# Performance work log

Measured on AMD Instinct MI355X. Metric: run time of the kernel, lower is better.

The kernel has to match this reference:

```python
import jax, jax.numpy as jnp
import numpy as np

ALPHA = 0.2      # LeakyReLU negative slope (hardcoded in StateNetwork: GAT(..., 0.2, 1))
MASK_FILL = 9e-15  # value used for non-edges BEFORE softmax (not -inf, per original code)

N_ENT = 4096     # len(vocab_kge): number of KG entities / GAT nodes
EMB = 64         # embedding_size == gat_emb_size
NHID = 3         # hardcoded in StateNetwork: GAT(gat_emb_size, 3, ...)
BATCH = 4        # number of graphs in graph_rep


def setup_inputs() -> dict:
    key = jax.random.key(0)
    k_adj, k_emb, k_W, k_a, k_fw, k_fb = jax.random.split(key, 6)
    adj = jax.random.randint(k_adj, (BATCH, N_ENT, N_ENT), 0, 2, dtype=jnp.int32)
    ent_emb = jax.random.normal(k_emb, (N_ENT, EMB), dtype=jnp.float32)
    W = jax.random.normal(k_W, (EMB, NHID), dtype=jnp.float32)
    a = jax.random.normal(k_a, (2 * NHID, 1), dtype=jnp.float32)
    fc1_w = jax.random.normal(k_fw, (100, N_ENT * NHID), dtype=jnp.float32) * 0.02
    fc1_b = jax.random.normal(k_fb, (100,), dtype=jnp.float32)
    return {"adj": adj, "ent_emb": ent_emb, "W": W, "a": a, "fc1_w": fc1_w, "fc1_b": fc1_b}


def reference(adj, ent_emb, W, a, fc1_w, fc1_b):
    # GAT layer over the shared entity-embedding node features (same for all graphs).
    h = ent_emb @ W                                   # [N, F]
    F_out = h.shape[1]
    # Pairwise concat score decomposes: e[i,j] = leakyrelu(a1.h_i + a2.h_j)
    src = h @ a[:F_out]                                # [N, 1]
    dst = h @ a[F_out:]                                # [N, 1]
    e = jax.nn.leaky_relu(src + dst.T, negative_slope=ALPHA)   # [N, N]
    # Masked softmax with 9e-15 fill (faithful to torch.where(adj>0, e, 9e-15))
    att = jnp.where(adj > 0, e[None, :, :], jnp.float32(MASK_FILL))  # [B, N, N]
    att = jax.nn.softmax(att, axis=-1)
    h_prime = jnp.einsum('bij,jf->bif', att, h)        # [B, N, F]
    x = jax.nn.elu(h_prime)                            # concat=True -> ELU
    x = x.reshape(adj.shape[0], -1)                    # [B, N*F]
    return x @ fc1_w.T + fc1_b                         # [B, 100]
```

## Files before the change

kernel.cpp:

```cpp
#include <hip/hip_runtime.h>
#include <math.h>

#define N_ENT 4096
#define BATCH 4
#define NHID  3
#define EMB   64
#define ALPHA 0.2f
#define MASK_FILL 9e-15f

__global__ __launch_bounds__(256) void prep_kernel(
    const float* __restrict__ emb, const float* __restrict__ W,
    const float* __restrict__ a,
    float* __restrict__ h0G, float* __restrict__ h1G, float* __restrict__ h2G,
    float* __restrict__ dstG, float* __restrict__ srcG)
{
    int j = blockIdx.x * 256 + threadIdx.x;
    if (j >= N_ENT) return;
    const float* er = emb + (size_t)j * EMB;
    float h0 = 0.f, h1 = 0.f, h2 = 0.f;
    #pragma unroll
    for (int e = 0; e < EMB; ++e) {
        float v = er[e];
        h0 += v * W[e * 3 + 0];
        h1 += v * W[e * 3 + 1];
        h2 += v * W[e * 3 + 2];
    }
    h0G[j] = h0; h1G[j] = h1; h2G[j] = h2;
    srcG[j] = h0 * a[0] + h1 * a[1] + h2 * a[2];
    dstG[j] = h0 * a[3] + h1 * a[4] + h2 * a[5];
}

__global__ __launch_bounds__(256, 2) void gat_row_kernel(
    const int* __restrict__ adj,
    const float* __restrict__ h0G, const float* __restrict__ h1G,
    const float* __restrict__ h2G, const float* __restrict__ dstG,
    const float* __restrict__ srcG, float* __restrict__ xG)
{
    __shared__ float dstL[N_ENT];
    __shared__ float h0L[N_ENT];
    __shared__ float h1L[N_ENT];
    __shared__ float h2L[N_ENT];

    int tid = threadIdx.x;
    for (int t = tid; t < N_ENT; t += 256) {
        dstL[t] = dstG[t];
        h0L[t]  = h0G[t];
        h1L[t]  = h1G[t];
        h2L[t]  = h2G[t];
    }
    __syncthreads();

    int lane = tid & 63;
    int gw   = blockIdx.x * 4 + (tid >> 6);

    for (int r = 0; r < 8; ++r) {
        int row = gw * 8 + r;
        int i   = row & (N_ENT - 1);
        float src = srcG[i];
        const int4* arow = (const int4*)(adj + (size_t)row * N_ENT);

        int4 av[16];
        #pragma unroll
        for (int c = 0; c < 16; ++c) av[c] = arow[c * 64 + lane];

        float vals[64];
        float m = -3.4e38f;
        #pragma unroll
        for (int c = 0; c < 16; ++c) {
            int jb = (c * 64 + lane) * 4;
            float4 d4 = *(const float4*)&dstL[jb];
            float t0 = src + d4.x, t1 = src + d4.y, t2 = src + d4.z, t3 = src + d4.w;
            float v0 = av[c].x > 0 ? fmaxf(t0, ALPHA * t0) : MASK_FILL;
            float v1 = av[c].y > 0 ? fmaxf(t1, ALPHA * t1) : MASK_FILL;
            float v2 = av[c].z > 0 ? fmaxf(t2, ALPHA * t2) : MASK_FILL;
            float v3 = av[c].w > 0 ? fmaxf(t3, ALPHA * t3) : MASK_FILL;
            vals[c * 4 + 0] = v0; vals[c * 4 + 1] = v1;
            vals[c * 4 + 2] = v2; vals[c * 4 + 3] = v3;
            m = fmaxf(m, fmaxf(fmaxf(v0, v1), fmaxf(v2, v3)));
        }
        #pragma unroll
        for (int off = 32; off; off >>= 1)
            m = fmaxf(m, __shfl_xor(m, off, 64));

        float l = 0.f, n0 = 0.f, n1 = 0.f, n2 = 0.f;
        #pragma unroll
        for (int c = 0; c < 16; ++c) {
            int jb = (c * 64 + lane) * 4;
            float4 a0 = *(const float4*)&h0L[jb];
            float4 a1 = *(const float4*)&h1L[jb];
            float4 a2 = *(const float4*)&h2L[jb];
            float p0 = __expf(vals[c * 4 + 0] - m);
            float p1 = __expf(vals[c * 4 + 1] - m);
            float p2 = __expf(vals[c * 4 + 2] - m);
            float p3 = __expf(vals[c * 4 + 3] - m);
            l  += (p0 + p1) + (p2 + p3);
            n0 += p0 * a0.x + p1 * a0.y + p2 * a0.z + p3 * a0.w;
            n1 += p0 * a1.x + p1 * a1.y + p2 * a1.z + p3 * a1.w;
            n2 += p0 * a2.x + p1 * a2.y + p2 * a2.z + p3 * a2.w;
        }
        #pragma unroll
        for (int off = 32; off; off >>= 1) {
            l  += __shfl_xor(l,  off, 64);
            n0 += __shfl_xor(n0, off, 64);
            n1 += __shfl_xor(n1, off, 64);
            n2 += __shfl_xor(n2, off, 64);
        }

        if (lane == 0) {
            float inv = 1.f / l;
            float hp0 = n0 * inv, hp1 = n1 * inv, hp2 = n2 * inv;
            float* xp = xG + (size_t)row * 3;
            xp[0] = hp0 > 0.f ? hp0 : expm1f(hp0);
            xp[1] = hp1 > 0.f ? hp1 : expm1f(hp1);
            xp[2] = hp2 > 0.f ? hp2 : expm1f(hp2);
        }
    }
}

__global__ __launch_bounds__(256) void fc_kernel(
    const float* __restrict__ xG, const float* __restrict__ w,
    const float* __restrict__ bias, float* __restrict__ out)
{
    int k   = blockIdx.x;
    int tid = threadIdx.x;
    const float4* wr = (const float4*)(w + (size_t)k * (N_ENT * NHID));
    const float4* x0 = (const float4*)(xG + 0 * (N_ENT * NHID));
    const float4* x1 = (const float4*)(xG + 1 * (N_ENT * NHID));
    const float4* x2 = (const float4*)(xG + 2 * (N_ENT * NHID));
    const float4* x3 = (const float4*)(xG + 3 * (N_ENT * NHID));

    float acc0 = 0.f, acc1 = 0.f, acc2 = 0.f, acc3 = 0.f;
    for (int t = tid; t < (N_ENT * NHID / 4); t += 256) {
        float4 wv = wr[t];
        float4 xv;
        xv = x0[t]; acc0 += wv.x*xv.x + wv.y*xv.y + wv.z*xv.z + wv.w*xv.w;
        xv = x1[t]; acc1 += wv.x*xv.x + wv.y*xv.y + wv.z*xv.z + wv.w*xv.w;
        xv = x2[t]; acc2 += wv.x*xv.x + wv.y*xv.y + wv.z*xv.z + wv.w*xv.w;
        xv = x3[t]; acc3 += wv.x*xv.x + wv.y*xv.y + wv.z*xv.z + wv.w*xv.w;
    }

    #pragma unroll
    for (int off = 32; off; off >>= 1) {
        acc0 += __shfl_xor(acc0, off, 64);
        acc1 += __shfl_xor(acc1, off, 64);
        acc2 += __shfl_xor(acc2, off, 64);
        acc3 += __shfl_xor(acc3, off, 64);
    }

    __shared__ float red[4][4];
    int lane = tid & 63, wv_ = tid >> 6;
    if (lane == 0) {
        red[wv_][0] = acc0; red[wv_][1] = acc1;
        red[wv_][2] = acc2; red[wv_][3] = acc3;
    }
    __syncthreads();
    if (tid < 4) {
        float s = red[0][tid] + red[1][tid] + red[2][tid] + red[3][tid] + bias[k];
        out[tid * 100 + k] = s;
    }
}

extern "C" void kernel_launch(void* const* d_in, const int* in_sizes, int n_in,
                              void* d_out, int out_size, void* d_ws, size_t ws_size,
                              hipStream_t stream)
{
    const int*   adj  = (const int*)d_in[0];
    const float* emb  = (const float*)d_in[1];
    const float* W    = (const float*)d_in[2];
    const float* a    = (const float*)d_in[3];
    const float* fc1w = (const float*)d_in[4];
    const float* fc1b = (const float*)d_in[5];
    float* out = (float*)d_out;

    float* ws   = (float*)d_ws;
    float* h0G  = ws;
    float* h1G  = ws + 4096;
    float* h2G  = ws + 8192;
    float* dstG = ws + 12288;
    float* srcG = ws + 16384;
    float* xG   = ws + 20480;

    prep_kernel<<<N_ENT / 256, 256, 0, stream>>>(emb, W, a, h0G, h1G, h2G, dstG, srcG);
    gat_row_kernel<<<512, 256, 0, stream>>>(adj, h0G, h1G, h2G, dstG, srcG, xG);
    fc_kernel<<<100, 256, 0, stream>>>(xG, fc1w, fc1b, out);
}
```

Before: 429.4 us.

## Replace two-pass masked softmax with single-pass online softmax per row

Switches the per-row softmax from a max pass followed by an exp/accumulate pass to an online softmax that rescales the running sum and numerators per chunk, then merges the per-lane (m, l, n) states across the wavefront with shuffles. This removes the 64-float vals array and the 16 int4 adjacency registers held across passes, which cuts register pressure. The cost is one extra exp and four rescales per chunk, plus extra exps in the cross-lane reduction. Adjacency loads are no longer all issued up front, so less memory-level parallelism is exposed per wave.

Result: faster. 410.0 us (-4.5%).

```diff
diff --git a/kernel.cpp b/kernel.cpp
--- a/kernel.cpp
+++ b/kernel.cpp
@@ -59,51 +59,54 @@
         float src = srcG[i];
         const int4* arow = (const int4*)(adj + (size_t)row * N_ENT);
 
-        int4 av[16];
-        #pragma unroll
-        for (int c = 0; c < 16; ++c) av[c] = arow[c * 64 + lane];
+        float m = -3.4e38f, l = 0.f, n0 = 0.f, n1 = 0.f, n2 = 0.f;
 
-        float vals[64];
-        float m = -3.4e38f;
-        #pragma unroll
+        #pragma unroll 4
         for (int c = 0; c < 16; ++c) {
+            int4 av = arow[c * 64 + lane];
             int jb = (c * 64 + lane) * 4;
             float4 d4 = *(const float4*)&dstL[jb];
+
             float t0 = src + d4.x, t1 = src + d4.y, t2 = src + d4.z, t3 = src + d4.w;
-            float v0 = av[c].x > 0 ? fmaxf(t0, ALPHA * t0) : MASK_FILL;
-            float v1 = av[c].y > 0 ? fmaxf(t1, ALPHA * t1) : MASK_FILL;
-            float v2 = av[c].z > 0 ? fmaxf(t2, ALPHA * t2) : MASK_FILL;
-            float v3 = av[c].w > 0 ? fmaxf(t3, ALPHA * t3) : MASK_FILL;
-            vals[c * 4 + 0] = v0; vals[c * 4 + 1] = v1;
-            vals[c * 4 + 2] = v2; vals[c * 4 + 3] = v3;
-            m = fmaxf(m, fmaxf(fmaxf(v0, v1), fmaxf(v2, v3)));
-        }
-        #pragma unroll
-        for (int off = 32; off; off >>= 1)
-            m = fmaxf(m, __shfl_xor(m, off, 64));
+            float v0 = av.x > 0 ? fmaxf(t0, ALPHA * t0) : MASK_FILL;
+            float v1 = av.y > 0 ? fmaxf(t1, ALPHA * t1) : MASK_FILL;
+            float v2 = av.z > 0 ? fmaxf(t2, ALPHA * t2) : MASK_FILL;
+            float v3 = av.w > 0 ? fmaxf(t3, ALPHA * t3) : MASK_FILL;
 
-        float l = 0.f, n0 = 0.f, n1 = 0.f, n2 = 0.f;
-        #pragma unroll
-        for (int c = 0; c < 16; ++c) {
-            int jb = (c * 64 + lane) * 4;
+            float m4 = fmaxf(fmaxf(v0, v1), fmaxf(v2, v3));
+            float mn = fmaxf(m, m4);
+            float s  = __expf(m - mn);
+            l *= s; n0 *= s; n1 *= s; n2 *= s;
+            m = mn;
+
             float4 a0 = *(const float4*)&h0L[jb];
             float4 a1 = *(const float4*)&h1L[jb];
             float4 a2 = *(const float4*)&h2L[jb];
-            float p0 = __expf(vals[c * 4 + 0] - m);
-            float p1 = __expf(vals[c * 4 + 1] - m);
-            float p2 = __expf(vals[c * 4 + 2] - m);
-            float p3 = __expf(vals[c * 4 + 3] - m);
+            float p0 = __expf(v0 - m);
+            float p1 = __expf(v1 - m);
+            float p2 = __expf(v2 - m);
+            float p3 = __expf(v3 - m);
             l  += (p0 + p1) + (p2 + p3);
             n0 += p0 * a0.x + p1 * a0.y + p2 * a0.z + p3 * a0.w;
             n1 += p0 * a1.x + p1 * a1.y + p2 * a1.z + p3 * a1.w;
             n2 += p0 * a2.x + p1 * a2.y + p2 * a2.z + p3 * a2.w;
         }
+
         #pragma unroll
         for (int off = 32; off; off >>= 1) {
-            l  += __shfl_xor(l,  off, 64);
-            n0 += __shfl_xor(n0, off, 64);
-            n1 += __shfl_xor(n1, off, 64);
-            n2 += __shfl_xor(n2, off, 64);
+            float mo = __shfl_xor(m,  off, 64);
+            float lo = __shfl_xor(l,  off, 64);
+            float o0 = __shfl_xor(n0, off, 64);
+            float o1 = __shfl_xor(n1, off, 64);
+            float o2 = __shfl_xor(n2, off, 64);
+            float mm = fmaxf(m, mo);
+            float sa = __expf(m  - mm);
+            float sb = __expf(mo - mm);
+            l  = l  * sa + lo * sb;
+            n0 = n0 * sa + o0 * sb;
+            n1 = n1 * sa + o1 * sb;
+            n2 = n2 * sa + o2 * sb;
+            m  = mm;
         }
 
         if (lane == 0) {
```

## Replace two-pass softmax with single-pass bound-max and exp2, widen blocks

Applied to the files above, without the earlier changes.

Instead of computing each row's exact max over the masked scores, the kernel takes an upper bound from the global max of dst (leaky-relu is monotonic), so the scores no longer have to be buffered and the loop becomes a single streaming pass that loads adj one chunk at a time. Scores are prescaled by log2(e) in prep so the loop can use the native exp2, and the masked entries use a precomputed constant. Blocks grow to 1024 threads with each wave handling 2 rows, which removes the large per-thread register arrays and raises occupancy. The trade-off is a smaller number of adj loads in flight per thread, and a loose max bound could cause exp underflow for some rows.

New measurement: 383.8 us. -10.6%, faster.

```diff
diff --git a/kernel.cpp b/kernel.cpp
--- a/kernel.cpp
+++ b/kernel.cpp
@@ -7,6 +7,18 @@
 #define EMB   64
 #define ALPHA 0.2f
 #define MASK_FILL 9e-15f
+#define LOG2E 1.4426950408889634f
+#define MASKP (MASK_FILL * LOG2E)
+
+#if defined(__has_builtin)
+#  if __has_builtin(__builtin_amdgcn_exp2f)
+#    define EXP2F(x) __builtin_amdgcn_exp2f(x)
+#  else
+#    define EXP2F(x) exp2f(x)
+#  endif
+#else
+#  define EXP2F(x) exp2f(x)
+#endif
 
 __global__ __launch_bounds__(256) void prep_kernel(
     const float* __restrict__ emb, const float* __restrict__ W,
@@ -26,11 +38,11 @@
         h2 += v * W[e * 3 + 2];
     }
     h0G[j] = h0; h1G[j] = h1; h2G[j] = h2;
-    srcG[j] = h0 * a[0] + h1 * a[1] + h2 * a[2];
-    dstG[j] = h0 * a[3] + h1 * a[4] + h2 * a[5];
-}
-
-__global__ __launch_bounds__(256, 2) void gat_row_kernel(
+    srcG[j] = (h0 * a[0] + h1 * a[1] + h2 * a[2]) * LOG2E;
+    dstG[j] = (h0 * a[3] + h1 * a[4] + h2 * a[5]) * LOG2E;
+}
+
+__global__ __launch_bounds__(1024, 8) void gat_row_kernel(
     const int* __restrict__ adj,
     const float* __restrict__ h0G, const float* __restrict__ h1G,
     const float* __restrict__ h2G, const float* __restrict__ dstG,
@@ -40,64 +52,67 @@
     __shared__ float h0L[N_ENT];
     __shared__ float h1L[N_ENT];
     __shared__ float h2L[N_ENT];
-
-    int tid = threadIdx.x;
-    for (int t = tid; t < N_ENT; t += 256) {
-        dstL[t] = dstG[t];
-        h0L[t]  = h0G[t];
-        h1L[t]  = h1G[t];
-        h2L[t]  = h2G[t];
-    }
+    __shared__ float maxdL[16];
+
+    int tid  = threadIdx.x;
+    int lane = tid & 63;
+    int wid  = tid >> 6;
+
+    float md = -3.4e38f;
+    #pragma unroll
+    for (int t = tid; t < N_ENT; t += 1024) {
+        float dv = dstG[t];
+        dstL[t] = dv;
+        md = fmaxf(md, dv);
+        h0L[t] = h0G[t];
+        h1L[t] = h1G[t];
+        h2L[t] = h2G[t];
+    }
+    #pragma unroll
+    for (int off = 32; off; off >>= 1) md = fmaxf(md, __shfl_xor(md, off, 64));
+    if (lane == 0) maxdL[wid] = md;
     __syncthreads();
-
-    int lane = tid & 63;
-    int gw   = blockIdx.x * 4 + (tid >> 6);
-
-    for (int r = 0; r < 8; ++r) {
-        int row = gw * 8 + r;
+    float maxd = maxdL[0];
+    #pragma unroll
+    for (int t = 1; t < 16; ++t) maxd = fmaxf(maxd, maxdL[t]);
+
+    int gw = blockIdx.x * 16 + wid;
+
+    for (int r = 0; r < 2; ++r) {
+        int row = gw * 2 + r;
         int i   = row & (N_ENT - 1);
-        float src = srcG[i];
+        float srcp = srcG[i];
+        float t0 = srcp + maxd;
+        float M  = fmaxf(fmaxf(t0, ALPHA * t0), (float)MASKP);
+        float sA = srcp - M;
+        float sB = ALPHA * srcp - M;
+        float CM = EXP2F((float)MASKP - M);
+
         const int4* arow = (const int4*)(adj + (size_t)row * N_ENT);
 
-        int4 av[16];
-        #pragma unroll
-        for (int c = 0; c < 16; ++c) av[c] = arow[c * 64 + lane];
-
-        float vals[64];
-        float m = -3.4e38f;
-        #pragma unroll
+        float l = 0.f, n0 = 0.f, n1 = 0.f, n2 = 0.f;
+        #pragma unroll 1
         for (int c = 0; c < 16; ++c) {
+            int4 av = arow[c * 64 + lane];
             int jb = (c * 64 + lane) * 4;
             float4 d4 = *(const float4*)&dstL[jb];
-            float t0 = src + d4.x, t1 = src + d4.y, t2 = src + d4.z, t3 = src + d4.w;
-            float v0 = av[c].x > 0 ? fmaxf(t0, ALPHA * t0) : MASK_FILL;
-            float v1 = av[c].y > 0 ? fmaxf(t1, ALPHA * t1) : MASK_FILL;
-            float v2 = av[c].z > 0 ? fmaxf(t2, ALPHA * t2) : MASK_FILL;
-            float v3 = av[c].w > 0 ? fmaxf(t3, ALPHA * t3) : MASK_FILL;
-            vals[c * 4 + 0] = v0; vals[c * 4 + 1] = v1;
-            vals[c * 4 + 2] = v2; vals[c * 4 + 3] = v3;
-            m = fmaxf(m, fmaxf(fmaxf(v0, v1), fmaxf(v2, v3)));
-        }
-        #pragma unroll
-        for (int off = 32; off; off >>= 1)
-            m = fmaxf(m, __shfl_xor(m, off, 64));
-
-        float l = 0.f, n0 = 0.f, n1 = 0.f, n2 = 0.f;
-        #pragma unroll
-        for (int c = 0; c < 16; ++c) {
-            int jb = (c * 64 + lane) * 4;
             float4 a0 = *(const float4*)&h0L[jb];
             float4 a1 = *(const float4*)&h1L[jb];
             float4 a2 = *(const float4*)&h2L[jb];
-            float p0 = __expf(vals[c * 4 + 0] - m);
-            float p1 = __expf(vals[c * 4 + 1] - m);
-            float p2 = __expf(vals[c * 4 + 2] - m);
-            float p3 = __expf(vals[c * 4 + 3] - m);
-            l  += (p0 + p1) + (p2 + p3);
-            n0 += p0 * a0.x + p1 * a0.y + p2 * a0.z + p3 * a0.w;
-            n1 += p0 * a1.x + p1 * a1.y + p2 * a1.z + p3 * a1.w;
-            n2 += p0 * a2.x + p1 * a2.y + p2 * a2.z + p3 * a2.w;
+            float g0 = EXP2F(fmaxf(sA + d4.x, fmaf(ALPHA, d4.x, sB)));
+            float g1 = EXP2F(fmaxf(sA + d4.y, fmaf(ALPHA, d4.y, sB)));
+            float g2 = EXP2F(fmaxf(sA + d4.z, fmaf(ALPHA, d4.z, sB)));
+            float g3 = EXP2F(fmaxf(sA + d4.w, fmaf(ALPHA, d4.w, sB)));
+            float w0 = av.x > 0 ? g0 : CM;
+            float w1 = av.y > 0 ? g1 : CM;
+            float w2 = av.z > 0 ? g2 : CM;
+            float w3 = av.w > 0 ? g3 : CM;
+            l  += (w0 + w1) + (w2 + w3);
+            n0 = fmaf(w0, a0.x, fmaf(w1, a0.y, fmaf(w2, a0.z, fmaf(w3, a0.w, n0))));
+            n1 = fmaf(w0, a1.x, fmaf(w1, a1.y, fmaf(w2, a1.z, fmaf(w3, a1.w, n1))));
+            n2 = fmaf(w0, a2.x, fmaf(w1, a2.y, fmaf(w2, a2.z, fmaf(w3, a2.w, n2))));
         }
+
         #pragma unroll
         for (int off = 32; off; off >>= 1) {
             l  += __shfl_xor(l,  off, 64);
@@ -181,6 +196,6 @@
     float* xG   = ws + 20480;
 
     prep_kernel<<<N_ENT / 256, 256, 0, stream>>>(emb, W, a, h0G, h1G, h2G, dstG, srcG);
-    gat_row_kernel<<<512, 256, 0, stream>>>(adj, h0G, h1G, h2G, dstG, srcG, xG);
+    gat_row_kernel<<<512, 1024, 0, stream>>>(adj, h0G, h1G, h2G, dstG, srcG, xG);
     fc_kernel<<<100, 256, 0, stream>>>(xG, fc1w, fc1b, out);
 }
```
